# Kernel optimization log

Hardware: AMD Instinct MI355X
Metric: run time of the kernel (lower is better)

Reference implementation:

```python
import jax, jax.numpy as jnp
import numpy as np

ALPHA = 0.2  # LeakyReLU negative slope
N, IN_DIM, OUT_DIM = 8192, 512, 64


def setup_inputs() -> dict:
    key = jax.random.key(0)
    k1, k2, k3, k4 = jax.random.split(key, 4)
    X = jax.random.normal(k1, (N, IN_DIM), dtype=jnp.float32)
    Adj = jax.random.randint(k2, (N, N), 0, 2, dtype=jnp.int32)
    # xavier_uniform with gain=1.414
    def xavier(k, shape, gain=1.414):
        fan_in, fan_out = shape[0], shape[1]
        bound = gain * np.sqrt(6.0 / (fan_in + fan_out))
        return jax.random.uniform(k, shape, jnp.float32, -bound, bound)
    W = xavier(k3, (IN_DIM, OUT_DIM))
    a = xavier(k4, (2 * OUT_DIM, 1))
    return {"X": X, "Adj": Adj, "W": W, "a": a}


def reference(X, Adj, W, a):
    # h = X @ W : [N, D]
    h = X @ W
    D = h.shape[1]
    # Decompose pairwise score: concat([h_i, h_j]) @ a == h_i @ a1 + h_j @ a2
    s1 = h @ a[:D, 0]   # [N] -- contribution of row (destination) node i
    s2 = h @ a[D:, 0]   # [N] -- contribution of column (source) node j
    e = jnp.exp(jax.nn.leaky_relu(s1[:, None] + s2[None, :], negative_slope=ALPHA))  # [N, N]
    e = jnp.where(Adj == 0, jnp.float32(0.0), e)
    attention = e / jnp.sum(e, axis=1, keepdims=True)
    # dropout is a no-op in eval mode (training=False)
    return attention @ h
```

## Files before the change

kernel.cpp:

```cpp
#include <hip/hip_runtime.h>
#include <math.h>


#define NN 8192
#define KIN 512
#define DD 64
#define ALPHA 0.2f

using floatx4 = __attribute__((ext_vector_type(4))) float;
using bf16x8  = __attribute__((ext_vector_type(8))) __bf16;
using bf16x4  = __attribute__((ext_vector_type(4))) __bf16;

__global__ __launch_bounds__(256) void k_gemm_h(const float* __restrict__ X,
                                                const float* __restrict__ W,
                                                float* __restrict__ h) {
    __shared__ __align__(16) float XT[32 * 36];
    __shared__ __align__(16) float WL[32 * 64];
    const int t = threadIdx.x;
    const int i0 = blockIdx.x * 32;
    const int rb = t >> 5;
    const int db = t & 31;
    float acc[4][2] = {};

    for (int k0 = 0; k0 < KIN; k0 += 32) {
        {
            const int row = t >> 3, kq = t & 7;
            const float4 x4 = *(const float4*)(X + (size_t)(i0 + row) * KIN + k0 + kq * 4);
            XT[(kq * 4 + 0) * 36 + row] = x4.x;
            XT[(kq * 4 + 1) * 36 + row] = x4.y;
            XT[(kq * 4 + 2) * 36 + row] = x4.z;
            XT[(kq * 4 + 3) * 36 + row] = x4.w;
#pragma unroll
            for (int p = 0; p < 2; ++p) {
                const int q = p * 256 + t;
                const int kk = q >> 4, dq = q & 15;
                *(float4*)(WL + kk * 64 + dq * 4) =
                    *(const float4*)(W + (size_t)(k0 + kk) * DD + dq * 4);
            }
        }
        __syncthreads();
#pragma unroll
        for (int k = 0; k < 32; ++k) {
            const float4 xa = *(const float4*)(XT + k * 36 + rb * 4);
            const float2 wb = *(const float2*)(WL + k * 64 + db * 2);
            const float xv[4] = {xa.x, xa.y, xa.z, xa.w};
#pragma unroll
            for (int i = 0; i < 4; ++i) {
                acc[i][0] += xv[i] * wb.x;
                acc[i][1] += xv[i] * wb.y;
            }
        }
        __syncthreads();
    }
#pragma unroll
    for (int i = 0; i < 4; ++i) {
        float2 o = {acc[i][0], acc[i][1]};
        *(float2*)(h + (size_t)(i0 + rb * 4 + i) * DD + db * 2) = o;
    }
}

__global__ __launch_bounds__(256) void k_s12(const float* __restrict__ h,
                                             const float* __restrict__ a,
                                             float* __restrict__ s1,
                                             float* __restrict__ s2) {
    const int lane = threadIdx.x & 63;
    const int w = threadIdx.x >> 6;
    const int r = blockIdx.x * 4 + w;
    const float v = h[(size_t)r * DD + lane];
    float p1 = v * a[lane];
    float p2 = v * a[64 + lane];
#pragma unroll
    for (int off = 32; off; off >>= 1) {
        p1 += __shfl_xor(p1, off, 64);
        p2 += __shfl_xor(p2, off, 64);
    }
    if (lane == 0) {
        s1[r] = p1;
        s2[r] = p2;
    }
}

__global__ __launch_bounds__(256) void k_hfrag(const float* __restrict__ h,
                                               __bf16* __restrict__ hFrag) {
    const int f = blockIdx.x * 256 + threadIdx.x;
    const int lane = f & 63, dt = (f >> 6) & 3, jblk = f >> 8;
    const int n = lane & 15, q = lane >> 4;
    bf16x8 v;
#pragma unroll
    for (int jj = 0; jj < 8; ++jj)
        v[jj] = (__bf16)h[(size_t)(jblk * 32 + q * 8 + jj) * DD + dt * 16 + n];
    *(bf16x8*)(hFrag + (size_t)f * 8) = v;
}

__global__ __launch_bounds__(256, 4) void k_attn3(const bf16x8* __restrict__ hFrag,
                                                  const int* __restrict__ Adj,
                                                  const float* __restrict__ s1,
                                                  const float* __restrict__ s2,
                                                  float* __restrict__ numP,
                                                  float* __restrict__ denP) {
    __shared__ __align__(16) __bf16 ET[4][16][264];
    const int t = threadIdx.x;
    const int wv = t >> 6;
    const int lane = t & 63;
    const int n = lane & 15, q = lane >> 4;
    const int it = blockIdx.x >> 3, jc = blockIdx.x & 7;
    const int i0 = it * 64;

    float s1v[16];
#pragma unroll
    for (int rr = 0; rr < 16; ++rr) s1v[rr] = s1[i0 + wv * 16 + rr];

    bf16x8 ones;
#pragma unroll
    for (int u = 0; u < 8; ++u) ones[u] = (__bf16)1.0f;

    floatx4 acc[5] = {};

    const int* adjBase = Adj + (size_t)(i0 + wv * 16) * NN + jc * 1024 + lane * 4;

    for (int w = 0; w < 4; ++w) {
        const int j0 = jc * 1024 + w * 256;
        const float4 z = *(const float4*)(s2 + j0 + lane * 4);
#pragma unroll
        for (int pass = 0; pass < 4; ++pass) {
            int4 av[4];
#pragma unroll
            for (int r4 = 0; r4 < 4; ++r4)
                av[r4] = *(const int4*)(adjBase + (size_t)(pass * 4 + r4) * NN + w * 256);
#pragma unroll
            for (int r4 = 0; r4 < 4; ++r4) {
                const int rr = pass * 4 + r4;
                const float s1r = s1v[rr];
                const int am[4] = {av[r4].x, av[r4].y, av[r4].z, av[r4].w};
                const float zz[4] = {z.x, z.y, z.z, z.w};
                bf16x4 ev;
#pragma unroll
                for (int c = 0; c < 4; ++c) {
                    const float s = s1r + zz[c];
                    const float l = fmaxf(s, ALPHA * s);
                    float e = __expf(l);
                    e = am[c] ? e : 0.f;
                    ev[c] = (__bf16)e;
                }
                *(bf16x4*)&ET[wv][rr][lane * 4] = ev;
            }
        }
        const int jblk0 = j0 >> 5;
#pragma unroll
        for (int ks = 0; ks < 8; ++ks) {
            const bf16x8 af = *(const bf16x8*)&ET[wv][n][ks * 32 + q * 8];
            const bf16x8* hf = hFrag + ((size_t)(jblk0 + ks) * 4) * 64 + lane;
#pragma unroll
            for (int dt = 0; dt < 4; ++dt)
                acc[dt] = __builtin_amdgcn_mfma_f32_16x16x32_bf16(af, hf[dt * 64], acc[dt], 0, 0, 0);
            acc[4] = __builtin_amdgcn_mfma_f32_16x16x32_bf16(af, ones, acc[4], 0, 0, 0);
        }
    }

    const size_t base = (size_t)blockIdx.x * 4096;
#pragma unroll
    for (int dt = 0; dt < 4; ++dt)
#pragma unroll
        for (int r = 0; r < 4; ++r)
            numP[base + (size_t)(wv * 16 + q * 4 + r) * 64 + dt * 16 + n] = acc[dt][r];

    if (n == 0) {
#pragma unroll
        for (int r = 0; r < 4; ++r)
            denP[(size_t)blockIdx.x * 64 + wv * 16 + q * 4 + r] = acc[4][r];
    }
}

__global__ __launch_bounds__(256) void k_final(const float* __restrict__ numP,
                                               const float* __restrict__ denP,
                                               float* __restrict__ out) {
    const int idx = blockIdx.x * 256 + threadIdx.x;
    const int i = idx >> 6, d = idx & 63;
    const int it = i >> 6, r = i & 63;
    float num = 0.f, den = 0.f;
#pragma unroll
    for (int c = 0; c < 8; ++c) {
        const size_t bx = (size_t)(it * 8 + c);
        num += numP[bx * 4096 + (size_t)r * 64 + d];
        den += denP[bx * 64 + r];
    }
    out[idx] = num / den;
}

extern "C" void kernel_launch(void* const* d_in, const int* in_sizes, int n_in,
                              void* d_out, int out_size, void* d_ws, size_t ws_size,
                              hipStream_t stream) {
    const float* X = (const float*)d_in[0];
    const int* Adj = (const int*)d_in[1];
    const float* W = (const float*)d_in[2];
    const float* a = (const float*)d_in[3];
    float* out = (float*)d_out;

    float* ws = (float*)d_ws;
    float* h = ws;
    float* s1 = h + 524288;
    float* s2 = s1 + 8192;
    __bf16* hFrag = (__bf16*)(s2 + 8192);
    float* numP = s2 + 8192 + 262144;
    float* denP = numP + 1024 * 4096;

    k_gemm_h<<<256, 256, 0, stream>>>(X, W, h);
    k_s12<<<2048, 256, 0, stream>>>(h, a, s1, s2);
    k_hfrag<<<256, 256, 0, stream>>>(h, hFrag);
    k_attn3<<<1024, 256, 0, stream>>>((const bf16x8*)hFrag, Adj, s1, s2, numP, denP);
    k_final<<<2048, 256, 0, stream>>>(numP, denP, out);
}
```

Before: 419.1 us.

## Bit-pack adjacency and build MFMA A-fragments directly in registers

```diff
diff --git a/kernel.cpp b/kernel.cpp
--- a/kernel.cpp
+++ b/kernel.cpp
@@ -9,7 +9,6 @@
 
 using floatx4 = __attribute__((ext_vector_type(4))) float;
 using bf16x8  = __attribute__((ext_vector_type(8))) __bf16;
-using bf16x4  = __attribute__((ext_vector_type(4))) __bf16;
 
 __global__ __launch_bounds__(256) void k_gemm_h(const float* __restrict__ X,
                                                 const float* __restrict__ W,
@@ -92,69 +91,82 @@
     *(bf16x8*)(hFrag + (size_t)f * 8) = v;
 }
 
-__global__ __launch_bounds__(256, 4) void k_attn3(const bf16x8* __restrict__ hFrag,
-                                                  const int* __restrict__ Adj,
+__global__ __launch_bounds__(256) void k_pack(const int* __restrict__ Adj,
+                                              unsigned int* __restrict__ mask) {
+    const int lane = threadIdx.x & 63;
+    const int wid = (blockIdx.x * 256 + threadIdx.x) >> 6;
+    const int nw = (gridDim.x * 256) >> 6;
+    for (int it = wid; it < (NN * NN / 512); it += nw) {
+        const size_t base = (size_t)it * 512;
+        unsigned long long m[8];
+#pragma unroll
+        for (int p = 0; p < 8; ++p) {
+            const int v = Adj[base + (size_t)p * 64 + lane];
+            m[p] = __ballot(v != 0);
+        }
+        if (lane == 0) {
+            unsigned long long* o = (unsigned long long*)mask + (size_t)it * 8;
+#pragma unroll
+            for (int p = 0; p < 8; ++p) o[p] = m[p];
+        }
+    }
+}
+
+__global__ __launch_bounds__(256, 4) void k_attn4(const bf16x8* __restrict__ hFrag,
+                                                  const unsigned int* __restrict__ mask,
                                                   const float* __restrict__ s1,
                                                   const float* __restrict__ s2,
                                                   float* __restrict__ numP,
                                                   float* __restrict__ denP) {
-    __shared__ __align__(16) __bf16 ET[4][16][264];
     const int t = threadIdx.x;
     const int wv = t >> 6;
     const int lane = t & 63;
     const int n = lane & 15, q = lane >> 4;
     const int it = blockIdx.x >> 3, jc = blockIdx.x & 7;
     const int i0 = it * 64;
-
-    float s1v[16];
-#pragma unroll
-    for (int rr = 0; rr < 16; ++rr) s1v[rr] = s1[i0 + wv * 16 + rr];
+    const int row = i0 + wv * 16 + n;
+    const float s1v = s1[row];
+
+    unsigned int mr[32];
+    {
+        const uint4* mp = (const uint4*)(mask + (size_t)row * 256 + jc * 32);
+#pragma unroll
+        for (int p = 0; p < 8; ++p) {
+            const uint4 v = mp[p];
+            mr[p * 4 + 0] = v.x;
+            mr[p * 4 + 1] = v.y;
+            mr[p * 4 + 2] = v.z;
+            mr[p * 4 + 3] = v.w;
+        }
+    }
 
     bf16x8 ones;
 #pragma unroll
     for (int u = 0; u < 8; ++u) ones[u] = (__bf16)1.0f;
 
     floatx4 acc[5] = {};
-
-    const int* adjBase = Adj + (size_t)(i0 + wv * 16) * NN + jc * 1024 + lane * 4;
-
-    for (int w = 0; w < 4; ++w) {
-        const int j0 = jc * 1024 + w * 256;
-        const float4 z = *(const float4*)(s2 + j0 + lane * 4);
-#pragma unroll
-        for (int pass = 0; pass < 4; ++pass) {
-            int4 av[4];
-#pragma unroll
-            for (int r4 = 0; r4 < 4; ++r4)
-                av[r4] = *(const int4*)(adjBase + (size_t)(pass * 4 + r4) * NN + w * 256);
-#pragma unroll
-            for (int r4 = 0; r4 < 4; ++r4) {
-                const int rr = pass * 4 + r4;
-                const float s1r = s1v[rr];
-                const int am[4] = {av[r4].x, av[r4].y, av[r4].z, av[r4].w};
-                const float zz[4] = {z.x, z.y, z.z, z.w};
-                bf16x4 ev;
-#pragma unroll
-                for (int c = 0; c < 4; ++c) {
-                    const float s = s1r + zz[c];
-                    const float l = fmaxf(s, ALPHA * s);
-                    float e = __expf(l);
-                    e = am[c] ? e : 0.f;
-                    ev[c] = (__bf16)e;
-                }
-                *(bf16x4*)&ET[wv][rr][lane * 4] = ev;
-            }
-        }
-        const int jblk0 = j0 >> 5;
-#pragma unroll
-        for (int ks = 0; ks < 8; ++ks) {
-            const bf16x8 af = *(const bf16x8*)&ET[wv][n][ks * 32 + q * 8];
-            const bf16x8* hf = hFrag + ((size_t)(jblk0 + ks) * 4) * 64 + lane;
-#pragma unroll
-            for (int dt = 0; dt < 4; ++dt)
-                acc[dt] = __builtin_amdgcn_mfma_f32_16x16x32_bf16(af, hf[dt * 64], acc[dt], 0, 0, 0);
-            acc[4] = __builtin_amdgcn_mfma_f32_16x16x32_bf16(af, ones, acc[4], 0, 0, 0);
-        }
+    const int jbase = jc * 1024;
+
+#pragma unroll
+    for (int ks = 0; ks < 32; ++ks) {
+        const int j0 = jbase + ks * 32 + q * 8;
+        const float4 z0 = *(const float4*)(s2 + j0);
+        const float4 z1 = *(const float4*)(s2 + j0 + 4);
+        const unsigned int bits = (mr[ks] >> (q * 8)) & 0xffu;
+        const float zz[8] = {z0.x, z0.y, z0.z, z0.w, z1.x, z1.y, z1.z, z1.w};
+        bf16x8 af;
+#pragma unroll
+        for (int u = 0; u < 8; ++u) {
+            const float s = s1v + zz[u];
+            const float l = fmaxf(s, ALPHA * s);
+            const float e = (bits & (1u << u)) ? __expf(l) : 0.f;
+            af[u] = (__bf16)e;
+        }
+        const bf16x8* hf = hFrag + ((size_t)(jc * 32 + ks) * 4) * 64 + lane;
+#pragma unroll
+        for (int dt = 0; dt < 4; ++dt)
+            acc[dt] = __builtin_amdgcn_mfma_f32_16x16x32_bf16(af, hf[dt * 64], acc[dt], 0, 0, 0);
+        acc[4] = __builtin_amdgcn_mfma_f32_16x16x32_bf16(af, ones, acc[4], 0, 0, 0);
     }
 
     const size_t base = (size_t)blockIdx.x * 4096;
@@ -201,12 +213,14 @@
     float* s1 = h + 524288;
     float* s2 = s1 + 8192;
     __bf16* hFrag = (__bf16*)(s2 + 8192);
-    float* numP = s2 + 8192 + 262144;
+    unsigned int* mask = (unsigned int*)(s2 + 8192 + 262144);
+    float* numP = s2 + 8192 + 262144 + 2097152;
     float* denP = numP + 1024 * 4096;
 
+    k_pack<<<2048, 256, 0, stream>>>(Adj, mask);
     k_gemm_h<<<256, 256, 0, stream>>>(X, W, h);
     k_s12<<<2048, 256, 0, stream>>>(h, a, s1, s2);
     k_hfrag<<<256, 256, 0, stream>>>(h, hFrag);
-    k_attn3<<<1024, 256, 0, stream>>>((const bf16x8*)hFrag, Adj, s1, s2, numP, denP);
+    k_attn4<<<1024, 256, 0, stream>>>((const bf16x8*)hFrag, mask, s1, s2, numP, denP);
     k_final<<<2048, 256, 0, stream>>>(numP, denP, out);
 }
```

Result: slower. 445.0 us (+6.2%).
